# Optimization experiments

Hardware: AMD Instinct MI355X
Metric: run time of the kernel (lower is better)

## Reference

```python
import jax, jax.numpy as jnp
import numpy as np

EPS_DIAG = 1e-4
EPS_SOFT = 1e-5
SCALE_DIV = 100000.0


def _cov2cor(x):
    # x: [N, C, d, d]; scale rows and cols by 1/sqrt(|diag|) (== D^-1 @ x @ D^-1)
    dia = jnp.abs(jnp.diagonal(x, axis1=-2, axis2=-1))          # [N, C, d]
    inv = 1.0 / jnp.sqrt(jnp.maximum(dia, EPS_DIAG))
    cor = x * inv[..., :, None] * inv[..., None, :]
    return jnp.clip(cor, -1.0, 1.0)


def _soft_pd_max(x):
    # x: [N, C, d, d]
    x = x - jnp.max(x, axis=(2, 3), keepdims=True)
    e = jnp.exp(x)
    dia = jnp.sum(e, axis=-1)                                    # [N, C, d]
    dia = jnp.maximum(dia, jnp.sum(dia, axis=2, keepdims=True) / SCALE_DIV)
    dia = jnp.maximum(dia, EPS_SOFT)
    inv = 1.0 / jnp.sqrt(dia)
    return e * inv[..., :, None] * inv[..., None, :]


def setup_inputs() -> dict:
    key = jax.random.key(0)
    k0, k1, k2, k3 = jax.random.split(key, 4)
    N, C, d = 64, 64, 64
    inputs = jax.random.normal(k0, (N, C, d, d), dtype=jnp.float32)
    # NonNeg uniform [0, 2/C] init for queries/keys
    w_queries = jax.random.uniform(k1, (C, C), dtype=jnp.float32, minval=0.0, maxval=2.0 / C)
    w_keys = jax.random.uniform(k2, (C, C), dtype=jnp.float32, minval=0.0, maxval=2.0 / C)
    # values: |N(0, 1/sqrt(C))| column-L1-normalized
    wv = jnp.abs(jax.random.normal(k3, (C, C), dtype=jnp.float32) / jnp.sqrt(jnp.float32(C)))
    w_values = wv / jnp.sum(wv, axis=0)
    return {"inputs": inputs, "w_queries": w_queries, "w_keys": w_keys, "w_values": w_values}


def reference(inputs, w_queries, w_keys, w_values):
    cor = _cov2cor(inputs)                                       # [N, C, d, d]
    X = jnp.transpose(cor, (0, 2, 3, 1))                         # [N, d, d, C]
    XWQ = jnp.matmul(X, w_queries)                               # [N, d, d, C]
    XWK = jnp.matmul(X, w_keys)
    XWV = jnp.matmul(X, w_values)
    XWQt = jnp.transpose(XWQ, (0, 3, 1, 2))                      # [N, C, d, d]
    XWKt = jnp.transpose(XWK, (0, 3, 2, 1))                      # [N, C, d, d] (transposed within dxd)
    XWKT = jnp.transpose(XWK, (0, 3, 1, 2))
    A_pre = jnp.matmul(jnp.matmul(XWKt, XWQt), XWKT)             # [N, C, d, d]
    A = _soft_pd_max(A_pre)
    V = jnp.transpose(XWV, (0, 3, 1, 2))                         # [N, C, d, d]
    AXA = jnp.matmul(jnp.matmul(A, V), jnp.transpose(A, (0, 1, 3, 2)))
    return inputs + AXA
```

## Files before the change

kernel.cpp:

```cpp
#include <hip/hip_runtime.h>

#define PITCH 72
#define QKV_STRIDE 12288

typedef __attribute__((ext_vector_type(8))) short short8v;
typedef __attribute__((ext_vector_type(4))) short short4v;
typedef __attribute__((ext_vector_type(4))) float f32x4;

__device__ __forceinline__ short f2bf(float v) {
    unsigned u = __builtin_bit_cast(unsigned, v);
    unsigned r = (u + 0x7FFFu + ((u >> 16) & 1u)) >> 16;
    return (short)r;
}
__device__ __forceinline__ float bf2f(short s) {
    unsigned u = ((unsigned)(unsigned short)s) << 16;
    return __builtin_bit_cast(float, u);
}

#define MFMA(a, b, c) __builtin_amdgcn_mfma_f32_16x16x32_bf16(a, b, c, 0, 0, 0)

__device__ __forceinline__ short8v ldfrag(const short* p, int rowtile, int kc, int l) {
    return *(const short8v*)&p[(rowtile * 16 + (l & 15)) * PITCH + kc * 32 + (l >> 4) * 8];
}
__device__ __forceinline__ short8v gfrag(const short* __restrict__ p, int rowtile, int kc, int l) {
    return *(const short8v*)&p[(rowtile * 16 + (l & 15)) * 64 + kc * 32 + (l >> 4) * 8];
}
__device__ __forceinline__ short8v gfrag_s(const short* __restrict__ p, int rowtile,
                                           int kc, int l, int stride) {
    return *(const short8v*)&p[(rowtile * 16 + (l & 15)) * stride + kc * 32 + (l >> 4) * 8];
}

__device__ __forceinline__ void p1(const short* xh, const short* yh,
                                   int w, int l, f32x4 (&acc)[4]) {
#pragma unroll
    for (int ct = 0; ct < 4; ++ct) acc[ct] = (f32x4){0.f, 0.f, 0.f, 0.f};
#pragma unroll
    for (int kc = 0; kc < 2; ++kc) {
        short8v aH = ldfrag(xh, w, kc, l);
#pragma unroll
        for (int ct = 0; ct < 4; ++ct)
            acc[ct] = MFMA(aH, ldfrag(yh, ct, kc, l), acc[ct]);
    }
}

__device__ __forceinline__ void p1_g(const short* __restrict__ xg, const short* yh,
                                     int w, int l, f32x4 (&acc)[4]) {
#pragma unroll
    for (int ct = 0; ct < 4; ++ct) acc[ct] = (f32x4){0.f, 0.f, 0.f, 0.f};
#pragma unroll
    for (int kc = 0; kc < 2; ++kc) {
        short8v aH = gfrag_s(xg, w, kc, l, QKV_STRIDE);
#pragma unroll
        for (int ct = 0; ct < 4; ++ct)
            acc[ct] = MFMA(aH, ldfrag(yh, ct, kc, l), acc[ct]);
    }
}

__device__ __forceinline__ void p2v_g(const short* __restrict__ xg,
                                      const short* yh, const short* yl,
                                      int w, int l, f32x4 (&acc)[4]) {
#pragma unroll
    for (int ct = 0; ct < 4; ++ct) acc[ct] = (f32x4){0.f, 0.f, 0.f, 0.f};
#pragma unroll
    for (int kc = 0; kc < 2; ++kc) {
        short8v aH = gfrag_s(xg, w, kc, l, QKV_STRIDE);
#pragma unroll
        for (int ct = 0; ct < 4; ++ct) {
            acc[ct] = MFMA(aH, ldfrag(yh, ct, kc, l), acc[ct]);
            acc[ct] = MFMA(aH, ldfrag(yl, ct, kc, l), acc[ct]);
        }
    }
}

__device__ __forceinline__ void p2a(const short* xh, const short* xl,
                                    const short* yh,
                                    int w, int l, f32x4 (&acc)[4]) {
#pragma unroll
    for (int ct = 0; ct < 4; ++ct) acc[ct] = (f32x4){0.f, 0.f, 0.f, 0.f};
#pragma unroll
    for (int kc = 0; kc < 2; ++kc) {
        short8v aH = ldfrag(xh, w, kc, l);
        short8v aL = ldfrag(xl, w, kc, l);
#pragma unroll
        for (int ct = 0; ct < 4; ++ct) {
            short8v bH = ldfrag(yh, ct, kc, l);
            acc[ct] = MFMA(aH, bH, acc[ct]);
            acc[ct] = MFMA(aL, bH, acc[ct]);
        }
    }
}

__device__ __forceinline__ void pack1(const f32x4 (&acc)[4], short* zh, int w, int l) {
    int m0 = w * 16 + (l >> 4) * 4;
#pragma unroll
    for (int ct = 0; ct < 4; ++ct) {
        int n = ct * 16 + (l & 15);
        short4v h;
#pragma unroll
        for (int r = 0; r < 4; ++r) h[r] = f2bf(acc[ct][r]);
        *(short4v*)&zh[n * PITCH + m0] = h;
    }
}

__device__ __forceinline__ void idtrans_ip1(short* pa, int w, int l) {
    short8v a0 = ldfrag(pa, w, 0, l);
    short8v a1 = ldfrag(pa, w, 1, l);
    short8v I0, I1;
#pragma unroll
    for (int j = 0; j < 8; ++j) {
        int bit = 8 * (l >> 4) + j;
        I0[j] = (bit == (l & 15))      ? (short)0x3F80 : (short)0;
        I1[j] = (bit == (l & 15) + 16) ? (short)0x3F80 : (short)0;
    }
    __syncthreads();
    int m0 = w * 16 + (l >> 4) * 4;
    const f32x4 z4 = {0.f, 0.f, 0.f, 0.f};
#pragma unroll
    for (int s = 0; s < 4; ++s) {
        f32x4 d = MFMA((s >> 1) ? a1 : a0, (s & 1) ? I1 : I0, z4);
        short4v ha;
#pragma unroll
        for (int r = 0; r < 4; ++r) ha[r] = f2bf(d[r]);
        *(short4v*)&pa[(s * 16 + (l & 15)) * PITCH + m0] = ha;
    }
}

__global__ __launch_bounds__(256) void k0_invdiag(const float* __restrict__ x,
                                                  float* __restrict__ invd) {
    int t = blockIdx.x * 256 + threadIdx.x;
    int nc = t >> 6, k = t & 63;
    float v = fabsf(x[(size_t)nc * 4096 + (size_t)k * 65]);
    invd[t] = rsqrtf(fmaxf(v, 1e-4f));
}

__global__ __launch_bounds__(256) void k0b_w3(const float* __restrict__ wq,
                                              const float* __restrict__ wk,
                                              const float* __restrict__ wv,
                                              short* __restrict__ w3h) {
    int idx = blockIdx.x * 256 + threadIdx.x;
    int co = idx >> 6, c = idx & 63;
    const float* w = (co < 64) ? wq : (co < 128) ? wk : wv;
    w3h[idx] = f2bf(w[c * 64 + (co & 63)]);
}

__global__ __launch_bounds__(256, 6) void k1_mix_mfma(
    const float* __restrict__ x, const float* __restrict__ invd,
    const short* __restrict__ w3h,
    short* __restrict__ QKV)
{
    __shared__ __align__(16) short ch[4608];

    const int b = blockIdx.x, n = b >> 6, i = b & 63;
    const int t = threadIdx.x, l = t & 63, w = t >> 6;
    const size_t nbase = (size_t)n * 64;

#pragma unroll
    for (int rep = 0; rep < 4; ++rep) {
        int id = rep * 256 + t;
        int c = id >> 4, j4 = (id & 15) * 4;
        float4 xv = *(const float4*)&x[((nbase + c) * 64 + i) * 64 + j4];
        float ii = invd[(nbase + c) * 64 + i];
        float4 jv = *(const float4*)&invd[(nbase + c) * 64 + j4];
        float vv[4] = {xv.x * ii * jv.x, xv.y * ii * jv.y,
                       xv.z * ii * jv.z, xv.w * ii * jv.w};
        short4v h;
#pragma unroll
        for (int r = 0; r < 4; ++r)
            h[r] = f2bf(fminf(1.0f, fmaxf(-1.0f, vv[r])));
        *(short4v*)&ch[c * PITCH + j4] = h;
    }
    __syncthreads();
    idtrans_ip1(ch, w, l);
    __syncthreads();

    f32x4 acc[4][3];
#pragma unroll
    for (int jt = 0; jt < 4; ++jt)
#pragma unroll
        for (int cc = 0; cc < 3; ++cc) acc[jt][cc] = (f32x4){0.f, 0.f, 0.f, 0.f};
#pragma unroll
    for (int kc = 0; kc < 2; ++kc) {
#pragma unroll
        for (int cc = 0; cc < 3; ++cc) {
            short8v bH = gfrag(w3h, w * 3 + cc, kc, l);
#pragma unroll
            for (int jt = 0; jt < 4; ++jt) {
                short8v aH = ldfrag(ch, jt, kc, l);
                acc[jt][cc] = MFMA(aH, bH, acc[jt][cc]);
            }
        }
    }

    {
        short* dst = QKV + (size_t)b * QKV_STRIDE;
        const int m0 = (l >> 4) * 4, nb = l & 15;
#pragma unroll
        for (int cc = 0; cc < 3; ++cc) {
            int nrow = (w * 3 + cc) * 16 + nb;
#pragma unroll
            for (int jt = 0; jt < 4; ++jt) {
                short4v h;
#pragma unroll
                for (int r = 0; r < 4; ++r) h[r] = f2bf(acc[jt][cc][r]);
                *(short4v*)&dst[nrow * 64 + jt * 16 + m0] = h;
            }
        }
    }
}

__global__ __launch_bounds__(256, 5) void k2_attn_mfma(
    const float* __restrict__ x,
    const short* __restrict__ QKV,
    float* __restrict__ out)
{
    __shared__ __align__(16) short P[3][4608];
    __shared__ float part[4][64];
    __shared__ float invs[64];
    __shared__ float red[4];

    const int t = threadIdx.x, l = t & 63, w = t >> 6;
    const int nc = blockIdx.x, n = nc >> 6, c = nc & 63;
    const size_t gbase = (size_t)nc * 4096;

    const short* qh = QKV + (size_t)n * 64 * QKV_STRIDE + (size_t)c * 64;
    const short* kh = qh + 64 * 64;
    const short* vh = qh + 128 * 64;

#pragma unroll
    for (int rep = 0; rep < 4; ++rep) {
        int id = rep * 256 + t;
        int r = id >> 4, c4 = (id & 15) * 4;
        *(short4v*)&P[0][r * PITCH + c4] =
            *(const short4v*)&kh[r * QKV_STRIDE + c4];
    }
    __syncthreads();

    idtrans_ip1(P[0], w, l);
    __syncthreads();

    f32x4 acc[4];

    p1_g(qh, P[0], w, l, acc);
    pack1(acc, P[1], w, l);
    __syncthreads();

    p1(P[1], P[0], w, l, acc);

    float mx = -1e30f;
#pragma unroll
    for (int ct = 0; ct < 4; ++ct)
#pragma unroll
        for (int r = 0; r < 4; ++r) mx = fmaxf(mx, acc[ct][r]);
#pragma unroll
    for (int off = 1; off < 64; off <<= 1) mx = fmaxf(mx, __shfl_xor(mx, off));
    if (l == 0) red[w] = mx;
    __syncthreads();
    mx = fmaxf(fmaxf(red[0], red[1]), fmaxf(red[2], red[3]));

    float e[4][4];
    float cs[4];
#pragma unroll
    for (int ct = 0; ct < 4; ++ct) {
        float s = 0.f;
#pragma unroll
        for (int r = 0; r < 4; ++r) {
            float ev = __expf(acc[ct][r] - mx);
            e[ct][r] = ev;
            s += ev;
        }
        cs[ct] = s;
    }
#pragma unroll
    for (int ct = 0; ct < 4; ++ct) {
        cs[ct] += __shfl_xor(cs[ct], 16);
        cs[ct] += __shfl_xor(cs[ct], 32);
    }
    if (l < 16) {
#pragma unroll
        for (int ct = 0; ct < 4; ++ct) part[w][ct * 16 + l] = cs[ct];
    }
    __syncthreads();
    if (t < 64) {
        float dia = part[0][t] + part[1][t] + part[2][t] + part[3][t];
        float tot = dia;
#pragma unroll
        for (int off = 1; off < 64; off <<= 1) tot += __shfl_xor(tot, off);
        dia = fmaxf(dia, tot / 100000.0f);
        dia = fmaxf(dia, 1e-5f);
        invs[t] = rsqrtf(dia);
    }
    __syncthreads();

    {
        int m0 = w * 16 + (l >> 4) * 4;
        float ir[4] = {invs[m0], invs[m0 + 1], invs[m0 + 2], invs[m0 + 3]};
        int nb = l & 15;
#pragma unroll
        for (int ct = 0; ct < 4; ++ct) {
            float ic = invs[ct * 16 + nb];
            short4v h, lo;
#pragma unroll
            for (int r = 0; r < 4; ++r) {
                float v = e[ct][r] * ir[r] * ic;
                short hb = f2bf(v);
                h[r]  = hb;
                lo[r] = f2bf(v - bf2f(hb));
            }
            *(short4v*)&P[1][(ct * 16 + nb) * PITCH + m0] = h;
            *(short4v*)&P[0][(ct * 16 + nb) * PITCH + m0] = lo;
        }
    }
    __syncthreads();

    p2v_g(vh, P[1], P[0], w, l, acc);
    pack1(acc, P[2], w, l);
    __syncthreads();

    p2a(P[1], P[0], P[2], w, l, acc);
    __syncthreads();

    {
        float* ofs = (float*)&P[0][0];
        int m0 = w * 16 + (l >> 4) * 4;
        int nb = l & 15;
#pragma unroll
        for (int ct = 0; ct < 4; ++ct)
#pragma unroll
            for (int r = 0; r < 4; ++r)
                ofs[(m0 + r) * 68 + ct * 16 + nb] = acc[ct][r];
    }
    __syncthreads();
    {
        const float* ofs = (const float*)&P[0][0];
#pragma unroll
        for (int rep = 0; rep < 4; ++rep) {
            int id = rep * 256 + t;
            int row = id >> 4, c4 = (id & 15) * 4;
            float4 v  = *(const float4*)&ofs[row * 68 + c4];
            float4 xv = *(const float4*)&x[gbase + (size_t)row * 64 + c4];
            *(float4*)&out[gbase + (size_t)row * 64 + c4] =
                make_float4(xv.x + v.x, xv.y + v.y, xv.z + v.z, xv.w + v.w);
        }
    }
}

extern "C" void kernel_launch(void* const* d_in, const int* in_sizes, int n_in,
                              void* d_out, int out_size, void* d_ws, size_t ws_size,
                              hipStream_t stream) {
    const float* x  = (const float*)d_in[0];
    const float* wq = (const float*)d_in[1];
    const float* wk = (const float*)d_in[2];
    const float* wv = (const float*)d_in[3];
    float* out = (float*)d_out;

    char* wsb = (char*)d_ws;
    float* invd = (float*)wsb;
    short* w3h  = (short*)(wsb + (1 << 20));
    short* QKV  = (short*)(wsb + (2 << 20));

    k0_invdiag<<<1024, 256, 0, stream>>>(x, invd);
    k0b_w3<<<48, 256, 0, stream>>>(wq, wk, wv, w3h);
    k1_mix_mfma<<<4096, 256, 0, stream>>>(x, invd, w3h, QKV);
    k2_attn_mfma<<<4096, 256, 0, stream>>>(x, QKV, out);
}
```

Before: 97.78 us.

## Drop bf16 hi/lo split in attention, fuse prep kernels, stage QKV stores

The attention kernel stops splitting the normalized softmax matrix into high and low bf16 parts, so the A·V and (AV)·Aᵀ products use single-bf16 MFMAs instead of two per tile. This also frees one LDS buffer and raises the occupancy hint. The two small prep kernels are merged into one launch. The mixing kernel now stages its QKV output through shared memory in two halves and writes it back as coalesced 16-byte stores, with a higher occupancy hint. Accuracy drops because the low-order correction term is gone.

```diff
diff --git a/kernel.cpp b/kernel.cpp
--- a/kernel.cpp
+++ b/kernel.cpp
@@ -56,40 +56,6 @@
     }
 }
 
-__device__ __forceinline__ void p2v_g(const short* __restrict__ xg,
-                                      const short* yh, const short* yl,
-                                      int w, int l, f32x4 (&acc)[4]) {
-#pragma unroll
-    for (int ct = 0; ct < 4; ++ct) acc[ct] = (f32x4){0.f, 0.f, 0.f, 0.f};
-#pragma unroll
-    for (int kc = 0; kc < 2; ++kc) {
-        short8v aH = gfrag_s(xg, w, kc, l, QKV_STRIDE);
-#pragma unroll
-        for (int ct = 0; ct < 4; ++ct) {
-            acc[ct] = MFMA(aH, ldfrag(yh, ct, kc, l), acc[ct]);
-            acc[ct] = MFMA(aH, ldfrag(yl, ct, kc, l), acc[ct]);
-        }
-    }
-}
-
-__device__ __forceinline__ void p2a(const short* xh, const short* xl,
-                                    const short* yh,
-                                    int w, int l, f32x4 (&acc)[4]) {
-#pragma unroll
-    for (int ct = 0; ct < 4; ++ct) acc[ct] = (f32x4){0.f, 0.f, 0.f, 0.f};
-#pragma unroll
-    for (int kc = 0; kc < 2; ++kc) {
-        short8v aH = ldfrag(xh, w, kc, l);
-        short8v aL = ldfrag(xl, w, kc, l);
-#pragma unroll
-        for (int ct = 0; ct < 4; ++ct) {
-            short8v bH = ldfrag(yh, ct, kc, l);
-            acc[ct] = MFMA(aH, bH, acc[ct]);
-            acc[ct] = MFMA(aL, bH, acc[ct]);
-        }
-    }
-}
-
 __device__ __forceinline__ void pack1(const f32x4 (&acc)[4], short* zh, int w, int l) {
     int m0 = w * 16 + (l >> 4) * 4;
 #pragma unroll
@@ -125,30 +91,33 @@
     }
 }
 
-__global__ __launch_bounds__(256) void k0_invdiag(const float* __restrict__ x,
-                                                  float* __restrict__ invd) {
-    int t = blockIdx.x * 256 + threadIdx.x;
-    int nc = t >> 6, k = t & 63;
-    float v = fabsf(x[(size_t)nc * 4096 + (size_t)k * 65]);
-    invd[t] = rsqrtf(fmaxf(v, 1e-4f));
-}
-
-__global__ __launch_bounds__(256) void k0b_w3(const float* __restrict__ wq,
-                                              const float* __restrict__ wk,
-                                              const float* __restrict__ wv,
-                                              short* __restrict__ w3h) {
-    int idx = blockIdx.x * 256 + threadIdx.x;
-    int co = idx >> 6, c = idx & 63;
-    const float* w = (co < 64) ? wq : (co < 128) ? wk : wv;
-    w3h[idx] = f2bf(w[c * 64 + (co & 63)]);
-}
-
-__global__ __launch_bounds__(256, 6) void k1_mix_mfma(
+__global__ __launch_bounds__(256) void k0_prep(const float* __restrict__ x,
+                                               const float* __restrict__ wq,
+                                               const float* __restrict__ wk,
+                                               const float* __restrict__ wv,
+                                               float* __restrict__ invd,
+                                               short* __restrict__ w3h) {
+    int b = blockIdx.x;
+    if (b < 1024) {
+        int t = b * 256 + threadIdx.x;
+        int nc = t >> 6, k = t & 63;
+        float v = fabsf(x[(size_t)nc * 4096 + (size_t)k * 65]);
+        invd[t] = rsqrtf(fmaxf(v, 1e-4f));
+    } else {
+        int idx = (b - 1024) * 256 + threadIdx.x;
+        int co = idx >> 6, c = idx & 63;
+        const float* w = (co < 64) ? wq : (co < 128) ? wk : wv;
+        w3h[idx] = f2bf(w[c * 64 + (co & 63)]);
+    }
+}
+
+__global__ __launch_bounds__(256, 8) void k1_mix_mfma(
     const float* __restrict__ x, const float* __restrict__ invd,
     const short* __restrict__ w3h,
     short* __restrict__ QKV)
 {
-    __shared__ __align__(16) short ch[4608];
+    __shared__ __align__(16) short smem[6912];
+    short* ch = smem;
 
     const int b = blockIdx.x, n = b >> 6, i = b & 63;
     const int t = threadIdx.x, l = t & 63, w = t >> 6;
@@ -190,30 +159,60 @@
             }
         }
     }
-
-    {
-        short* dst = QKV + (size_t)b * QKV_STRIDE;
-        const int m0 = (l >> 4) * 4, nb = l & 15;
+    __syncthreads();
+
+    const int m0 = (l >> 4) * 4, nb = l & 15;
+    short* dst = QKV + (size_t)b * QKV_STRIDE;
+
+    if (w < 2) {
 #pragma unroll
         for (int cc = 0; cc < 3; ++cc) {
-            int nrow = (w * 3 + cc) * 16 + nb;
+            int zrow = (w * 3 + cc) * 16 + nb;
 #pragma unroll
             for (int jt = 0; jt < 4; ++jt) {
                 short4v h;
 #pragma unroll
                 for (int r = 0; r < 4; ++r) h[r] = f2bf(acc[jt][cc][r]);
-                *(short4v*)&dst[nrow * 64 + jt * 16 + m0] = h;
+                *(short4v*)&smem[zrow * PITCH + jt * 16 + m0] = h;
             }
         }
     }
-}
-
-__global__ __launch_bounds__(256, 5) void k2_attn_mfma(
+    __syncthreads();
+#pragma unroll
+    for (int rep = 0; rep < 3; ++rep) {
+        int id = rep * 256 + t;
+        *(short8v*)&dst[id * 8] = *(short8v*)&smem[(id >> 3) * PITCH + (id & 7) * 8];
+    }
+    __syncthreads();
+
+    if (w >= 2) {
+#pragma unroll
+        for (int cc = 0; cc < 3; ++cc) {
+            int zrow = ((w - 2) * 3 + cc) * 16 + nb;
+#pragma unroll
+            for (int jt = 0; jt < 4; ++jt) {
+                short4v h;
+#pragma unroll
+                for (int r = 0; r < 4; ++r) h[r] = f2bf(acc[jt][cc][r]);
+                *(short4v*)&smem[zrow * PITCH + jt * 16 + m0] = h;
+            }
+        }
+    }
+    __syncthreads();
+#pragma unroll
+    for (int rep = 0; rep < 3; ++rep) {
+        int id = rep * 256 + t;
+        *(short8v*)&dst[6144 + id * 8] =
+            *(short8v*)&smem[(id >> 3) * PITCH + (id & 7) * 8];
+    }
+}
+
+__global__ __launch_bounds__(256, 6) void k2_attn_mfma(
     const float* __restrict__ x,
     const short* __restrict__ QKV,
     float* __restrict__ out)
 {
-    __shared__ __align__(16) short P[3][4608];
+    __shared__ __align__(16) short P[2][4608];
     __shared__ float part[4][64];
     __shared__ float invs[64];
     __shared__ float red[4];
@@ -298,25 +297,20 @@
 #pragma unroll
         for (int ct = 0; ct < 4; ++ct) {
             float ic = invs[ct * 16 + nb];
-            short4v h, lo;
-#pragma unroll
-            for (int r = 0; r < 4; ++r) {
-                float v = e[ct][r] * ir[r] * ic;
-                short hb = f2bf(v);
-                h[r]  = hb;
-                lo[r] = f2bf(v - bf2f(hb));
-            }
+            short4v h;
+#pragma unroll
+            for (int r = 0; r < 4; ++r)
+                h[r] = f2bf(e[ct][r] * ir[r] * ic);
             *(short4v*)&P[1][(ct * 16 + nb) * PITCH + m0] = h;
-            *(short4v*)&P[0][(ct * 16 + nb) * PITCH + m0] = lo;
-        }
-    }
-    __syncthreads();
-
-    p2v_g(vh, P[1], P[0], w, l, acc);
-    pack1(acc, P[2], w, l);
-    __syncthreads();
-
-    p2a(P[1], P[0], P[2], w, l, acc);
+        }
+    }
+    __syncthreads();
+
+    p1_g(vh, P[1], w, l, acc);
+    pack1(acc, P[0], w, l);
+    __syncthreads();
+
+    p1(P[1], P[0], w, l, acc);
     __syncthreads();
 
     {
@@ -358,8 +352,7 @@
     short* w3h  = (short*)(wsb + (1 << 20));
     short* QKV  = (short*)(wsb + (2 << 20));
 
-    k0_invdiag<<<1024, 256, 0, stream>>>(x, invd);
-    k0b_w3<<<48, 256, 0, stream>>>(wq, wk, wv, w3h);
+    k0_prep<<<1072, 256, 0, stream>>>(x, wq, wk, wv, invd, w3h);
     k1_mix_mfma<<<4096, 256, 0, stream>>>(x, invd, w3h, QKV);
     k2_attn_mfma<<<4096, 256, 0, stream>>>(x, QKV, out);
 }
```

Measured after the change: 173.2 us. +77.1%, slower.
